# Kernel tuning notes

Hardware: AMD Instinct MI355X
Metric: run time of the kernel (lower is better)

Reference implementation:

```python
import jax, jax.numpy as jnp
import numpy as np

N_NODES = 100000
N_EDGES = 1000000

def _gcn_conv(x, W, b, src, dst, n_nodes):
    # PyG GCNConv: linear first, then symmetric-normalized aggregation with self loops
    x = x @ W  # [N, F_out]
    loop = jnp.arange(n_nodes, dtype=src.dtype)
    src2 = jnp.concatenate([src, loop])
    dst2 = jnp.concatenate([dst, loop])
    deg = jax.ops.segment_sum(jnp.ones(src2.shape[0], x.dtype), dst2, num_segments=n_nodes)
    dinv = jnp.where(deg > 0, jax.lax.rsqrt(deg), 0.0)
    norm = dinv[src2] * dinv[dst2]  # [E+N]
    msgs = x[src2] * norm[:, None]  # gather + scale
    out = jax.ops.segment_sum(msgs, dst2, num_segments=n_nodes)  # scatter-add
    return out + b

def _pair_norm_si(x):
    # mode 'PN-SI', scale=1
    x = x - x.mean(axis=0)
    row_norm = jnp.sqrt(1e-6 + jnp.sum(x * x, axis=1, keepdims=True))
    return x / row_norm

def setup_inputs() -> dict:
    key = jax.random.key(0)
    k1, k2, k3, k4 = jax.random.split(key, 4)
    in_c, hid_c, out_c = 256, 64, 40
    x = jax.random.normal(k1, (N_NODES, in_c), dtype=jnp.float32)
    edge_index = jax.random.randint(k2, (2, N_EDGES), 0, N_NODES, dtype=jnp.int64)
    W1 = jax.random.normal(k3, (in_c, hid_c), dtype=jnp.float32) / np.sqrt(in_c)
    b1 = jnp.zeros((hid_c,), jnp.float32)
    W2 = jax.random.normal(k4, (hid_c, out_c), dtype=jnp.float32) / np.sqrt(hid_c)
    b2 = jnp.zeros((out_c,), jnp.float32)
    return {"x": x, "edge_index": edge_index, "W1": W1, "b1": b1, "W2": W2, "b2": b2}

def reference(x, edge_index, W1, b1, W2, b2):
    src, dst = edge_index[0], edge_index[1]
    n = x.shape[0]
    h = jax.nn.relu(_gcn_conv(x, W1, b1, src, dst, n))
    h = _gcn_conv(h, W2, b2, src, dst, n)
    h = _pair_norm_si(h)
    return jax.nn.log_softmax(h, axis=1)
```

## Files before the change

### kernel.cpp

```cpp
#include <hip/hip_runtime.h>
#include <hip/hip_fp16.h>
#include <math.h>

#define F_IN  256
#define F_HID 64
#define F_OUT 40
#define HS2_LD 64

typedef _Float16 h8 __attribute__((ext_vector_type(8)));
typedef _Float16 h4 __attribute__((ext_vector_type(4)));
typedef float f4 __attribute__((ext_vector_type(4)));

__global__ void k_deg(const int* __restrict__ dst, unsigned* __restrict__ degc, int E) {
    int i = blockIdx.x * blockDim.x + threadIdx.x;
    if (i < E) atomicAdd(&degc[dst[i]], 1u);
}

__global__ __launch_bounds__(256) void k_scanA(const unsigned* __restrict__ degc,
                                               unsigned* __restrict__ exscan,
                                               unsigned* __restrict__ bsum, int N) {
    __shared__ unsigned s[256];
    int tid = threadIdx.x;
    int i = blockIdx.x * 256 + tid;
    unsigned v = (i < N) ? ((degc[i] + 8u) & ~7u) : 0u;
    s[tid] = v;
    __syncthreads();
    for (int off = 1; off < 256; off <<= 1) {
        unsigned t = (tid >= off) ? s[tid - off] : 0u;
        __syncthreads();
        s[tid] += t;
        __syncthreads();
    }
    if (i < N) exscan[i] = s[tid] - v;
    if (tid == 255) bsum[blockIdx.x] = s[255];
}

__global__ __launch_bounds__(512) void k_scanB(unsigned* __restrict__ bsum, int nb) {
    __shared__ unsigned s[512];
    int tid = threadIdx.x;
    unsigned v = (tid < nb) ? bsum[tid] : 0u;
    s[tid] = v;
    __syncthreads();
    for (int off = 1; off < 512; off <<= 1) {
        unsigned t = (tid >= off) ? s[tid - off] : 0u;
        __syncthreads();
        s[tid] += t;
        __syncthreads();
    }
    if (tid < nb) bsum[tid] = s[tid] - v;
}

__global__ void k_scanC(const unsigned* __restrict__ degc, const unsigned* __restrict__ exscan,
                        const unsigned* __restrict__ bsum, unsigned* __restrict__ rowptr,
                        float* __restrict__ dinv, int N) {
    int i = blockIdx.x * blockDim.x + threadIdx.x;
    if (i < N) {
        unsigned rp = exscan[i] + bsum[i >> 8];
        rowptr[i] = rp;
        dinv[i] = rsqrtf((float)degc[i] + 1.0f);
        if (i == N - 1) rowptr[N] = rp + ((degc[i] + 8u) & ~7u);
        if (i == 0) dinv[N] = 1.0f;
    }
}

__global__ void k_fill(const int* __restrict__ src, const int* __restrict__ dst,
                       const unsigned* __restrict__ rowptr, unsigned* __restrict__ cursor,
                       unsigned* __restrict__ colp, int E) {
    int e = blockIdx.x * blockDim.x + threadIdx.x;
    if (e >= E) return;
    int d = dst[e];
    unsigned p = atomicAdd(&cursor[d], 1u);
    colp[rowptr[d] + p] = (unsigned)src[e];
}

__global__ void k_pad(const unsigned* __restrict__ degc, const unsigned* __restrict__ rowptr,
                      unsigned* __restrict__ colp, int N) {
    int i = blockIdx.x * blockDim.x + threadIdx.x;
    if (i >= N) return;
    unsigned d = degc[i];
    unsigned base = rowptr[i];
    unsigned pd = (d + 8u) & ~7u;
    colp[base + d] = (unsigned)i;
    for (unsigned p = d + 1; p < pd; ++p) colp[base + p] = (unsigned)N;
}

__global__ void k_wt(const float* __restrict__ W1, __half* __restrict__ Wt) {
    int i = blockIdx.x * 256 + threadIdx.x;
    int k = i >> 6, n = i & 63;
    Wt[n * 256 + k] = __float2half(W1[i]);
}

#define XS 136
__global__ __launch_bounds__(256) void k_mm1(const float* __restrict__ x,
                                             const __half* __restrict__ Wth,
                                             const float* __restrict__ dinv,
                                             __half* __restrict__ hs1o, int N) {
    __shared__ _Float16 sX[64 * XS];
    const _Float16* Wt = (const _Float16*)Wth;
    _Float16* hs1 = (_Float16*)hs1o;
    int tid = threadIdx.x;
    int lane = tid & 63;
    int wv = tid >> 6;
    int m15 = lane & 15;
    int q = lane >> 4;
    int nbase = blockIdx.x * 64;

    h8 bf[8];
    #pragma unroll
    for (int kt = 0; kt < 8; ++kt)
        bf[kt] = *(const h8*)(Wt + (wv * 16 + m15) * 256 + kt * 32 + q * 8);

    f4 acc[4];
    #pragma unroll
    for (int mt = 0; mt < 4; ++mt) acc[mt] = (f4){0.f, 0.f, 0.f, 0.f};

    #pragma unroll
    for (int c = 0; c < 2; ++c) {
        #pragma unroll
        for (int p = 0; p < 8; ++p) {
            int idx = p * 256 + tid;
            int row = idx >> 5;
            int c4  = idx & 31;
            int node = nbase + row;
            float4 v = (node < N) ? *(const float4*)(x + (size_t)node * F_IN + c * 128 + c4 * 4)
                                  : make_float4(0.f, 0.f, 0.f, 0.f);
            h4 hv = { (_Float16)v.x, (_Float16)v.y, (_Float16)v.z, (_Float16)v.w };
            *(h4*)&sX[row * XS + c4 * 4] = hv;
        }
        __syncthreads();
        #pragma unroll
        for (int kt2 = 0; kt2 < 4; ++kt2) {
            #pragma unroll
            for (int mt = 0; mt < 4; ++mt) {
                h8 a = *(const h8*)&sX[(mt * 16 + m15) * XS + kt2 * 32 + q * 8];
                acc[mt] = __builtin_amdgcn_mfma_f32_16x16x32_f16(a, bf[c * 4 + kt2], acc[mt], 0, 0, 0);
            }
        }
        __syncthreads();
    }

    #pragma unroll
    for (int mt = 0; mt < 4; ++mt) {
        #pragma unroll
        for (int r = 0; r < 4; ++r) {
            int node = nbase + mt * 16 + q * 4 + r;
            if (node <= N) {
                float din = (node < N) ? dinv[node] : 1.0f;
                hs1[(size_t)node * F_HID + wv * 16 + m15] = (_Float16)(acc[mt][r] * din);
            }
        }
    }
}

__global__ __launch_bounds__(256) void k_agg1(const unsigned* __restrict__ rowptr,
                                              const unsigned* __restrict__ colp,
                                              const float* __restrict__ dinv,
                                              const __half* __restrict__ hs1o,
                                              const float* __restrict__ bias1,
                                              float* __restrict__ agg1, int N) {
    const _Float16* hp = (const _Float16*)hs1o;
    int lane = threadIdx.x & 63;
    int w = blockIdx.x * 4 + (threadIdx.x >> 6);
    int na = 2 * w, nb = 2 * w + 1;
    if (na >= N) return;
    int g = lane >> 3, c = lane & 7;

    float accA[8], accB[8];
    #pragma unroll
    for (int j = 0; j < 8; ++j) { accA[j] = 0.f; accB[j] = 0.f; }

    unsigned aE = rowptr[na], aEnd = rowptr[na + 1];
    bool hasB = (nb < N);
    unsigned bE = 0, bEnd = 0;
    if (hasB) { bE = rowptr[nb]; bEnd = rowptr[nb + 1]; }

    while (aE < aEnd && bE < bEnd) {
        unsigned sA = colp[aE + g];
        unsigned sB = colp[bE + g];
        h8 va = *(const h8*)(hp + (size_t)sA * F_HID + c * 8);
        h8 vb = *(const h8*)(hp + (size_t)sB * F_HID + c * 8);
        #pragma unroll
        for (int j = 0; j < 8; ++j) { accA[j] += (float)va[j]; accB[j] += (float)vb[j]; }
        aE += 8; bE += 8;
    }
    while (aE < aEnd) {
        unsigned sA = colp[aE + g];
        h8 va = *(const h8*)(hp + (size_t)sA * F_HID + c * 8);
        #pragma unroll
        for (int j = 0; j < 8; ++j) accA[j] += (float)va[j];
        aE += 8;
    }
    while (bE < bEnd) {
        unsigned sB = colp[bE + g];
        h8 vb = *(const h8*)(hp + (size_t)sB * F_HID + c * 8);
        #pragma unroll
        for (int j = 0; j < 8; ++j) accB[j] += (float)vb[j];
        bE += 8;
    }

    #pragma unroll
    for (int off = 8; off <= 32; off <<= 1) {
        #pragma unroll
        for (int j = 0; j < 8; ++j) {
            accA[j] += __shfl_xor(accA[j], off, 64);
            accB[j] += __shfl_xor(accB[j], off, 64);
        }
    }

    if (g == 0) {
        float4 b0 = *(const float4*)(bias1 + c * 8);
        float4 b1v = *(const float4*)(bias1 + c * 8 + 4);
        float dinA = dinv[na];
        float4 o0, o1;
        o0.x = fmaxf(accA[0] * dinA + b0.x, 0.f); o0.y = fmaxf(accA[1] * dinA + b0.y, 0.f);
        o0.z = fmaxf(accA[2] * dinA + b0.z, 0.f); o0.w = fmaxf(accA[3] * dinA + b0.w, 0.f);
        o1.x = fmaxf(accA[4] * dinA + b1v.x, 0.f); o1.y = fmaxf(accA[5] * dinA + b1v.y, 0.f);
        o1.z = fmaxf(accA[6] * dinA + b1v.z, 0.f); o1.w = fmaxf(accA[7] * dinA + b1v.w, 0.f);
        *(float4*)(agg1 + (size_t)na * F_HID + c * 8) = o0;
        *(float4*)(agg1 + (size_t)na * F_HID + c * 8 + 4) = o1;
        if (hasB) {
            float dinB = dinv[nb];
            o0.x = fmaxf(accB[0] * dinB + b0.x, 0.f); o0.y = fmaxf(accB[1] * dinB + b0.y, 0.f);
            o0.z = fmaxf(accB[2] * dinB + b0.z, 0.f); o0.w = fmaxf(accB[3] * dinB + b0.w, 0.f);
            o1.x = fmaxf(accB[4] * dinB + b1v.x, 0.f); o1.y = fmaxf(accB[5] * dinB + b1v.y, 0.f);
            o1.z = fmaxf(accB[6] * dinB + b1v.z, 0.f); o1.w = fmaxf(accB[7] * dinB + b1v.w, 0.f);
            *(float4*)(agg1 + (size_t)nb * F_HID + c * 8) = o0;
            *(float4*)(agg1 + (size_t)nb * F_HID + c * 8 + 4) = o1;
        }
    }
}

__global__ __launch_bounds__(512) void k_mm2(const float* __restrict__ a,
                                             const float* __restrict__ W2,
                                             const float* __restrict__ dinv,
                                             __half* __restrict__ hs2, int N) {
    __shared__ float sW[F_HID * 64];
    int tid = threadIdx.x;
    for (int idx = tid; idx < F_HID * 64; idx += 512) {
        int k = idx >> 6, f = idx & 63;
        sW[idx] = (f < F_OUT) ? W2[k * F_OUT + f] : 0.f;
    }
    __syncthreads();

    int f = tid & 63, r = tid >> 6;
    int node = blockIdx.x * 8 + r;
    if (node > N) return;
    const float* ar = a + (size_t)node * F_HID;
    float acc = 0.f;
    #pragma unroll 8
    for (int k = 0; k < F_HID; ++k) acc = fmaf(ar[k], sW[k * 64 + f], acc);
    float val = (node < N) ? acc * dinv[node] : 0.f;
    hs2[(size_t)node * HS2_LD + f] = __float2half(val);
}

__global__ __launch_bounds__(256) void k_agg2(const unsigned* __restrict__ rowptr,
                                              const unsigned* __restrict__ colp,
                                              const float* __restrict__ dinv,
                                              const __half* __restrict__ hs2o,
                                              float* __restrict__ out,
                                              float* __restrict__ colsum, int N) {
    __shared__ float part[4][8][8];
    const _Float16* hp = (const _Float16*)hs2o;
    int lane = threadIdx.x & 63;
    int wv = threadIdx.x >> 6;
    int g = lane >> 3, c = lane & 7;
    int nwaves = gridDim.x * 4;
    float csum[8];
    #pragma unroll
    for (int j = 0; j < 8; ++j) csum[j] = 0.f;

    for (int w = blockIdx.x * 4 + wv; 2 * w < N; w += nwaves) {
        int na = 2 * w, nb = 2 * w + 1;
        float accA[8], accB[8];
        #pragma unroll
        for (int j = 0; j < 8; ++j) { accA[j] = 0.f; accB[j] = 0.f; }

        unsigned aE = rowptr[na], aEnd = rowptr[na + 1];
        bool hasB = (nb < N);
        unsigned bE = 0, bEnd = 0;
        if (hasB) { bE = rowptr[nb]; bEnd = rowptr[nb + 1]; }

        while (aE < aEnd && bE < bEnd) {
            unsigned sA = colp[aE + g];
            unsigned sB = colp[bE + g];
            h8 va = *(const h8*)(hp + (size_t)sA * HS2_LD + c * 8);
            h8 vb = *(const h8*)(hp + (size_t)sB * HS2_LD + c * 8);
            #pragma unroll
            for (int j = 0; j < 8; ++j) { accA[j] += (float)va[j]; accB[j] += (float)vb[j]; }
            aE += 8; bE += 8;
        }
        while (aE < aEnd) {
            unsigned sA = colp[aE + g];
            h8 va = *(const h8*)(hp + (size_t)sA * HS2_LD + c * 8);
            #pragma unroll
            for (int j = 0; j < 8; ++j) accA[j] += (float)va[j];
            aE += 8;
        }
        while (bE < bEnd) {
            unsigned sB = colp[bE + g];
            h8 vb = *(const h8*)(hp + (size_t)sB * HS2_LD + c * 8);
            #pragma unroll
            for (int j = 0; j < 8; ++j) accB[j] += (float)vb[j];
            bE += 8;
        }

        #pragma unroll
        for (int off = 8; off <= 32; off <<= 1) {
            #pragma unroll
            for (int j = 0; j < 8; ++j) {
                accA[j] += __shfl_xor(accA[j], off, 64);
                accB[j] += __shfl_xor(accB[j], off, 64);
            }
        }

        if (g == 0) {
            float dinA = dinv[na];
            #pragma unroll
            for (int j = 0; j < 8; ++j) { accA[j] *= dinA; csum[j] += accA[j]; }
            if (c < 5) {
                *(float4*)(out + (size_t)na * F_OUT + c * 8) =
                    make_float4(accA[0], accA[1], accA[2], accA[3]);
                *(float4*)(out + (size_t)na * F_OUT + c * 8 + 4) =
                    make_float4(accA[4], accA[5], accA[6], accA[7]);
            }
            if (hasB) {
                float dinB = dinv[nb];
                #pragma unroll
                for (int j = 0; j < 8; ++j) { accB[j] *= dinB; csum[j] += accB[j]; }
                if (c < 5) {
                    *(float4*)(out + (size_t)nb * F_OUT + c * 8) =
                        make_float4(accB[0], accB[1], accB[2], accB[3]);
                    *(float4*)(out + (size_t)nb * F_OUT + c * 8 + 4) =
                        make_float4(accB[4], accB[5], accB[6], accB[7]);
                }
            }
        }
    }

    if (g == 0) {
        #pragma unroll
        for (int j = 0; j < 8; ++j) part[wv][c][j] = csum[j];
    }
    __syncthreads();
    int tid = threadIdx.x;
    if (tid < F_OUT) {
        int cc = tid >> 3, jj = tid & 7;
        float s = part[0][cc][jj] + part[1][cc][jj] + part[2][cc][jj] + part[3][cc][jj];
        atomicAdd(&colsum[tid], s);
    }
}

__global__ __launch_bounds__(128) void k_final(float* __restrict__ out,
                                               const float* __restrict__ colsum, int N) {
    __shared__ float sMean[F_OUT];
    if (threadIdx.x < F_OUT) sMean[threadIdx.x] = colsum[threadIdx.x] * (1.0f / (float)N);
    __syncthreads();
    int n = blockIdx.x * blockDim.x + threadIdx.x;
    if (n >= N) return;
    float* row = out + (size_t)n * F_OUT;
    float v[F_OUT];
    float ss = 0.f;
    #pragma unroll
    for (int f = 0; f < F_OUT; ++f) {
        float t = row[f] - sMean[f];
        v[f] = t;
        ss += t * t;
    }
    float scale = 1.0f / sqrtf(ss + 1e-6f);
    float m = -1e30f;
    #pragma unroll
    for (int f = 0; f < F_OUT; ++f) {
        float y = v[f] * scale;
        v[f] = y;
        m = fmaxf(m, y);
    }
    float sum = 0.f;
    #pragma unroll
    for (int f = 0; f < F_OUT; ++f) sum += expf(v[f] - m);
    float lse = logf(sum);
    #pragma unroll
    for (int f = 0; f < F_OUT; ++f) row[f] = v[f] - m - lse;
}

extern "C" void kernel_launch(void* const* d_in, const int* in_sizes, int n_in,
                              void* d_out, int out_size, void* d_ws, size_t ws_size,
                              hipStream_t stream) {
    const float* x  = (const float*)d_in[0];
    const int*   ei = (const int*)d_in[1];
    const float* W1 = (const float*)d_in[2];
    const float* b1 = (const float*)d_in[3];
    const float* W2 = (const float*)d_in[4];
    float* out = (float*)d_out;

    int N = in_sizes[0] / F_IN;
    int E = in_sizes[1] / 2;
    const int* src = ei;
    const int* dst = ei + E;

    char* p = (char*)d_ws;
    auto alloc = [&](size_t bytes) { char* r = p; p += (bytes + 127) & ~(size_t)127; return r; };
    unsigned* degc   = (unsigned*)alloc((size_t)N * 4);
    unsigned* cursor = (unsigned*)alloc((size_t)N * 4);
    float*    colsum = (float*)   alloc(64 * 4);
    unsigned* rowptr = (unsigned*)alloc((size_t)(N + 1) * 4);
    unsigned* colp   = (unsigned*)alloc((size_t)(E + 8 * N + 8) * 4);
    float*    dinv   = (float*)   alloc((size_t)(N + 1) * 4);
    float*    agg1   = (float*)   alloc((size_t)64 * (N + 1) * 4);
    __half*   hs1    = (__half*)  alloc((size_t)64 * (N + 1) * 2);
    __half*   hs2    = (__half*)  alloc((size_t)64 * (N + 1) * 2);
    __half*   Wt     = (__half*)  alloc((size_t)16384 * 2);
    unsigned* exscan = (unsigned*)agg1;
    unsigned* bsum   = exscan + N;

    hipMemsetAsync(d_ws, 0, (char*)(colsum + 64) - (char*)d_ws, stream);

    int nA = (N + 255) / 256;
    k_deg<<<(E + 255) / 256, 256, 0, stream>>>(dst, degc, E);
    k_scanA<<<nA, 256, 0, stream>>>(degc, exscan, bsum, N);
    k_scanB<<<1, 512, 0, stream>>>(bsum, nA);
    k_scanC<<<nA, 256, 0, stream>>>(degc, exscan, bsum, rowptr, dinv, N);
    k_fill<<<(E + 255) / 256, 256, 0, stream>>>(src, dst, rowptr, cursor, colp, E);
    k_pad<<<nA, 256, 0, stream>>>(degc, rowptr, colp, N);
    k_wt<<<64, 256, 0, stream>>>(W1, Wt);
    k_mm1<<<(N + 63) / 64, 256, 0, stream>>>(x, Wt, dinv, hs1, N);
    int waves1 = (N + 1) / 2;
    k_agg1<<<(waves1 + 3) / 4, 256, 0, stream>>>(rowptr, colp, dinv, hs1, b1, agg1, N);
    k_mm2<<<(N + 8) / 8, 512, 0, stream>>>(agg1, W2, dinv, hs2, N);
    k_agg2<<<2048, 256, 0, stream>>>(rowptr, colp, dinv, hs2, out, colsum, N);
    k_final<<<(N + 127) / 128, 128, 0, stream>>>(out, colsum, N);
}
```

Baseline: 461.9 us.

## Store layer-1 activations in fp16 and compute second matmul with MFMA

The first aggregation now writes its ReLU output as fp16 instead of fp32, which halves that intermediate's write and read traffic. The second linear layer is rewritten from a scalar FMA loop with LDS weights into a 16x16x32 fp16 MFMA kernel. It stages 64-node tiles in padded shared memory and reads a pre-transposed fp16 W2 produced by a new small kernel. This adds fp16 rounding of hidden activations and one extra tiny launch.

Measured after the change: 404.8 us. -12.4%, faster.

```diff
diff --git a/kernel.cpp b/kernel.cpp
--- a/kernel.cpp
+++ b/kernel.cpp
@@ -88,6 +88,12 @@
     int i = blockIdx.x * 256 + threadIdx.x;
     int k = i >> 6, n = i & 63;
     Wt[n * 256 + k] = __float2half(W1[i]);
+}
+
+__global__ void k_w2t(const float* __restrict__ W2, __half* __restrict__ W2t) {
+    int i = blockIdx.x * 256 + threadIdx.x;
+    int n = i >> 6, k = i & 63;
+    W2t[n * 64 + k] = __float2half((n < F_OUT) ? W2[k * F_OUT + n] : 0.f);
 }
 
 #define XS 136
@@ -157,8 +163,9 @@
                                               const float* __restrict__ dinv,
                                               const __half* __restrict__ hs1o,
                                               const float* __restrict__ bias1,
-                                              float* __restrict__ agg1, int N) {
+                                              __half* __restrict__ agg1o, int N) {
     const _Float16* hp = (const _Float16*)hs1o;
+    _Float16* agg1h = (_Float16*)agg1o;
     int lane = threadIdx.x & 63;
     int w = blockIdx.x * 4 + (threadIdx.x >> 6);
     int na = 2 * w, nb = 2 * w + 1;
@@ -208,49 +215,80 @@
     }
 
     if (g == 0) {
-        float4 b0 = *(const float4*)(bias1 + c * 8);
-        float4 b1v = *(const float4*)(bias1 + c * 8 + 4);
+        float bv[8];
+        *(float4*)&bv[0] = *(const float4*)(bias1 + c * 8);
+        *(float4*)&bv[4] = *(const float4*)(bias1 + c * 8 + 4);
         float dinA = dinv[na];
-        float4 o0, o1;
-        o0.x = fmaxf(accA[0] * dinA + b0.x, 0.f); o0.y = fmaxf(accA[1] * dinA + b0.y, 0.f);
-        o0.z = fmaxf(accA[2] * dinA + b0.z, 0.f); o0.w = fmaxf(accA[3] * dinA + b0.w, 0.f);
-        o1.x = fmaxf(accA[4] * dinA + b1v.x, 0.f); o1.y = fmaxf(accA[5] * dinA + b1v.y, 0.f);
-        o1.z = fmaxf(accA[6] * dinA + b1v.z, 0.f); o1.w = fmaxf(accA[7] * dinA + b1v.w, 0.f);
-        *(float4*)(agg1 + (size_t)na * F_HID + c * 8) = o0;
-        *(float4*)(agg1 + (size_t)na * F_HID + c * 8 + 4) = o1;
+        h8 ho;
+        #pragma unroll
+        for (int j = 0; j < 8; ++j) ho[j] = (_Float16)fmaxf(accA[j] * dinA + bv[j], 0.f);
+        *(h8*)(agg1h + (size_t)na * F_HID + c * 8) = ho;
         if (hasB) {
             float dinB = dinv[nb];
-            o0.x = fmaxf(accB[0] * dinB + b0.x, 0.f); o0.y = fmaxf(accB[1] * dinB + b0.y, 0.f);
-            o0.z = fmaxf(accB[2] * dinB + b0.z, 0.f); o0.w = fmaxf(accB[3] * dinB + b0.w, 0.f);
-            o1.x = fmaxf(accB[4] * dinB + b1v.x, 0.f); o1.y = fmaxf(accB[5] * dinB + b1v.y, 0.f);
-            o1.z = fmaxf(accB[6] * dinB + b1v.z, 0.f); o1.w = fmaxf(accB[7] * dinB + b1v.w, 0.f);
-            *(float4*)(agg1 + (size_t)nb * F_HID + c * 8) = o0;
-            *(float4*)(agg1 + (size_t)nb * F_HID + c * 8 + 4) = o1;
-        }
-    }
-}
-
-__global__ __launch_bounds__(512) void k_mm2(const float* __restrict__ a,
-                                             const float* __restrict__ W2,
+            #pragma unroll
+            for (int j = 0; j < 8; ++j) ho[j] = (_Float16)fmaxf(accB[j] * dinB + bv[j], 0.f);
+            *(h8*)(agg1h + (size_t)nb * F_HID + c * 8) = ho;
+        }
+    }
+}
+
+#define AS 72
+__global__ __launch_bounds__(256) void k_mm2(const __half* __restrict__ agg1o,
+                                             const __half* __restrict__ W2th,
                                              const float* __restrict__ dinv,
-                                             __half* __restrict__ hs2, int N) {
-    __shared__ float sW[F_HID * 64];
+                                             __half* __restrict__ hs2o, int N) {
+    __shared__ _Float16 sA[64 * AS];
+    const _Float16* agg1h = (const _Float16*)agg1o;
+    const _Float16* W2t = (const _Float16*)W2th;
+    _Float16* hs2 = (_Float16*)hs2o;
     int tid = threadIdx.x;
-    for (int idx = tid; idx < F_HID * 64; idx += 512) {
-        int k = idx >> 6, f = idx & 63;
-        sW[idx] = (f < F_OUT) ? W2[k * F_OUT + f] : 0.f;
+    int lane = tid & 63;
+    int wv = tid >> 6;
+    int m15 = lane & 15;
+    int q = lane >> 4;
+    int nbase = blockIdx.x * 64;
+
+    h8 bf[2];
+    #pragma unroll
+    for (int kt = 0; kt < 2; ++kt)
+        bf[kt] = *(const h8*)(W2t + (wv * 16 + m15) * 64 + kt * 32 + q * 8);
+
+    #pragma unroll
+    for (int p = 0; p < 2; ++p) {
+        int idx = p * 256 + tid;
+        int row = idx >> 3;
+        int c8  = idx & 7;
+        int node = nbase + row;
+        h8 v;
+        if (node < N) v = *(const h8*)(agg1h + (size_t)node * F_HID + c8 * 8);
+        else          v = (h8){0, 0, 0, 0, 0, 0, 0, 0};
+        *(h8*)&sA[row * AS + c8 * 8] = v;
     }
     __syncthreads();
 
-    int f = tid & 63, r = tid >> 6;
-    int node = blockIdx.x * 8 + r;
-    if (node > N) return;
-    const float* ar = a + (size_t)node * F_HID;
-    float acc = 0.f;
-    #pragma unroll 8
-    for (int k = 0; k < F_HID; ++k) acc = fmaf(ar[k], sW[k * 64 + f], acc);
-    float val = (node < N) ? acc * dinv[node] : 0.f;
-    hs2[(size_t)node * HS2_LD + f] = __float2half(val);
+    f4 acc[4];
+    #pragma unroll
+    for (int mt = 0; mt < 4; ++mt) acc[mt] = (f4){0.f, 0.f, 0.f, 0.f};
+    #pragma unroll
+    for (int kt = 0; kt < 2; ++kt) {
+        #pragma unroll
+        for (int mt = 0; mt < 4; ++mt) {
+            h8 a = *(const h8*)&sA[(mt * 16 + m15) * AS + kt * 32 + q * 8];
+            acc[mt] = __builtin_amdgcn_mfma_f32_16x16x32_f16(a, bf[kt], acc[mt], 0, 0, 0);
+        }
+    }
+
+    #pragma unroll
+    for (int mt = 0; mt < 4; ++mt) {
+        #pragma unroll
+        for (int r = 0; r < 4; ++r) {
+            int node = nbase + mt * 16 + q * 4 + r;
+            if (node <= N) {
+                float din = (node < N) ? dinv[node] : 1.0f;
+                hs2[(size_t)node * HS2_LD + wv * 16 + m15] = (_Float16)(acc[mt][r] * din);
+            }
+        }
+    }
 }
 
 __global__ __launch_bounds__(256) void k_agg2(const unsigned* __restrict__ rowptr,
@@ -405,11 +443,12 @@
     unsigned* rowptr = (unsigned*)alloc((size_t)(N + 1) * 4);
     unsigned* colp   = (unsigned*)alloc((size_t)(E + 8 * N + 8) * 4);
     float*    dinv   = (float*)   alloc((size_t)(N + 1) * 4);
-    float*    agg1   = (float*)   alloc((size_t)64 * (N + 1) * 4);
+    __half*   agg1h  = (__half*)  alloc((size_t)64 * (N + 1) * 2);
     __half*   hs1    = (__half*)  alloc((size_t)64 * (N + 1) * 2);
     __half*   hs2    = (__half*)  alloc((size_t)64 * (N + 1) * 2);
     __half*   Wt     = (__half*)  alloc((size_t)16384 * 2);
-    unsigned* exscan = (unsigned*)agg1;
+    __half*   W2t    = (__half*)  alloc((size_t)4096 * 2);
+    unsigned* exscan = (unsigned*)agg1h;
     unsigned* bsum   = exscan + N;
 
     hipMemsetAsync(d_ws, 0, (char*)(colsum + 64) - (char*)d_ws, stream);
@@ -422,10 +461,11 @@
     k_fill<<<(E + 255) / 256, 256, 0, stream>>>(src, dst, rowptr, cursor, colp, E);
     k_pad<<<nA, 256, 0, stream>>>(degc, rowptr, colp, N);
     k_wt<<<64, 256, 0, stream>>>(W1, Wt);
+    k_w2t<<<16, 256, 0, stream>>>(W2, W2t);
     k_mm1<<<(N + 63) / 64, 256, 0, stream>>>(x, Wt, dinv, hs1, N);
     int waves1 = (N + 1) / 2;
-    k_agg1<<<(waves1 + 3) / 4, 256, 0, stream>>>(rowptr, colp, dinv, hs1, b1, agg1, N);
-    k_mm2<<<(N + 8) / 8, 512, 0, stream>>>(agg1, W2, dinv, hs2, N);
+    k_agg1<<<(waves1 + 3) / 4, 256, 0, stream>>>(rowptr, colp, dinv, hs1, b1, agg1h, N);
+    k_mm2<<<(N + 64) / 64, 256, 0, stream>>>(agg1h, W2t, dinv, hs2, N);
     k_agg2<<<2048, 256, 0, stream>>>(rowptr, colp, dinv, hs2, out, colsum, N);
     k_final<<<(N + 127) / 128, 128, 0, stream>>>(out, colsum, N);
 }
```
